# Performance work log

Measured on AMD Instinct MI355X. Metric: run time of the kernel, lower is better.

## Reference

```python
import jax, jax.numpy as jnp
import numpy as np

# static config (matches init_kwargs)
H = 64; W = 64; WS = 8; SHIFT = 4; HEADS = 16; DIM = 512; TED = 512; B = 16
NW = (H // WS) * (W // WS)          # 64 windows
WS2 = WS * WS                        # 64 tokens per window
N = WS2 + 1                          # +1 time-embedding token appended per window
HIDDEN = int(DIM * 4.0)


def _rel_pos_index():
    # standard Swin relative-position index over the WS*WS window tokens
    coords = np.stack(np.meshgrid(np.arange(WS), np.arange(WS), indexing='ij'))  # (2, WS, WS)
    cf = coords.reshape(2, -1)
    rel = (cf[:, :, None] - cf[:, None, :]).transpose(1, 2, 0)  # (WS2, WS2, 2)
    rel[..., 0] += WS - 1
    rel[..., 1] += WS - 1
    rel[..., 0] *= 2 * WS - 1
    return rel.sum(-1)  # (WS2, WS2) int


def _attn_mask():
    # shifted-window attention mask, exactly as built in __init__
    img_mask = np.zeros((H, W), dtype=np.float32)
    slices = (slice(0, -WS), slice(-WS, -SHIFT), slice(-SHIFT, None))
    cnt = 0
    for hs in slices:
        for ws_ in slices:
            img_mask[hs, ws_] = cnt
            cnt += 1
    mw = img_mask.reshape(H // WS, WS, W // WS, WS).transpose(0, 2, 1, 3).reshape(-1, WS2)  # (NW, WS2)
    diff = mw[:, None, :] - mw[:, :, None]
    return np.where(diff != 0, -100.0, 0.0).astype(np.float32)  # (NW, WS2, WS2)


def _ln(x, g, b):
    m = x.mean(-1, keepdims=True)
    v = ((x - m) ** 2).mean(-1, keepdims=True)
    return (x - m) / jnp.sqrt(v + 1e-5) * g + b


def setup_inputs() -> dict:
    key = jax.random.key(0)
    ks = jax.random.split(key, 10)
    s = 0.02
    return {
        'x': jax.random.normal(ks[0], (B, H * W, DIM), dtype=jnp.float32),
        'emb': jax.random.normal(ks[1], (B, TED), dtype=jnp.float32),
        'gamma1': jnp.ones((DIM,), jnp.float32),
        'beta1': jnp.zeros((DIM,), jnp.float32),
        'W_emb': jax.random.normal(ks[2], (TED, DIM), jnp.float32) * s,
        'b_emb': jnp.zeros((DIM,), jnp.float32),
        'W_qkv': jax.random.normal(ks[3], (DIM, 3 * DIM), jnp.float32) * s,
        'b_qkv': jnp.zeros((3 * DIM,), jnp.float32),
        'rel_bias_table': jax.random.normal(ks[4], ((2 * WS - 1) ** 2, HEADS), jnp.float32) * s,
        'W_proj': jax.random.normal(ks[5], (DIM, DIM), jnp.float32) * s,
        'b_proj': jnp.zeros((DIM,), jnp.float32),
        'gamma2': jnp.ones((DIM,), jnp.float32),
        'beta2': jnp.zeros((DIM,), jnp.float32),
        'W1': jax.random.normal(ks[6], (DIM, HIDDEN), jnp.float32) * s,
        'b1': jnp.zeros((HIDDEN,), jnp.float32),
        'W2': jax.random.normal(ks[7], (HIDDEN, DIM), jnp.float32) * s,
        'b2': jnp.zeros((DIM,), jnp.float32),
    }


def reference(x, emb, gamma1, beta1, W_emb, b_emb, W_qkv, b_qkv, rel_bias_table,
              W_proj, b_proj, gamma2, beta2, W1, b1, W2, b2):
    Bb, L, C = x.shape
    hd = C // HEADS
    shortcut = x
    # norm1 -> spatial -> cyclic shift
    xn = _ln(x, gamma1, beta1).reshape(Bb, H, W, C)
    xs = jnp.roll(xn, (-SHIFT, -SHIFT), axis=(1, 2))
    # window partition: (B, NW, WS2, C)
    xw = xs.reshape(Bb, H // WS, WS, W // WS, WS, C).transpose(0, 1, 3, 2, 4, 5)
    xw = xw.reshape(Bb, NW, WS2, C)
    # append time-embedding token to each window
    t = jax.nn.silu(emb) @ W_emb + b_emb                       # (B, C)
    t = jnp.broadcast_to(t[:, None, None, :], (Bb, NW, 1, C))
    xw = jnp.concatenate([xw, t], axis=2).reshape(Bb * NW, N, C)
    # windowed multi-head attention
    qkv = (xw @ W_qkv + b_qkv).reshape(Bb * NW, N, 3, HEADS, hd).transpose(2, 0, 3, 1, 4)
    q, k, v = qkv[0] * (hd ** -0.5), qkv[1], qkv[2]            # (B*NW, HEADS, N, hd)
    attn = jnp.einsum('bhnd,bhmd->bhnm', q, k)
    bias = rel_bias_table[_rel_pos_index().reshape(-1)].reshape(WS2, WS2, HEADS).transpose(2, 0, 1)
    bias = jnp.pad(bias, ((0, 0), (0, 1), (0, 1)))             # zero bias for time token
    attn = attn + bias[None]
    mask = jnp.pad(jnp.asarray(_attn_mask()), ((0, 0), (0, 1), (0, 1)))  # (NW, N, N)
    attn = attn.reshape(Bb, NW, HEADS, N, N) + mask[None, :, None]
    attn = jax.nn.softmax(attn.reshape(Bb * NW, HEADS, N, N), axis=-1)
    out = jnp.einsum('bhnm,bhmd->bnhd', attn, v).reshape(Bb * NW, N, C)
    out = (out @ W_proj + b_proj)[:, :WS2]                     # drop time token
    # window reverse + reverse shift
    out = out.reshape(Bb, H // WS, W // WS, WS, WS, C).transpose(0, 1, 3, 2, 4, 5).reshape(Bb, H, W, C)
    out = jnp.roll(out, (SHIFT, SHIFT), axis=(1, 2)).reshape(Bb, L, C)
    x1 = shortcut + out
    # norm2 + MLP (exact GELU, as torch nn.GELU default)
    hmid = jax.nn.gelu(_ln(x1, gamma2, beta2) @ W1 + b1, approximate=False)
    return x1 + hmid @ W2 + b2
```

## Files before the change

kernel.cpp:

```cpp
#include <hip/hip_runtime.h>
#include <hip/hip_bf16.h>

typedef __hip_bfloat16 bf16;
typedef short short4_t __attribute__((ext_vector_type(4)));
typedef short short8 __attribute__((ext_vector_type(8)));
typedef float f32x4 __attribute__((ext_vector_type(4)));

#define DIMC 512
#define HEADS_ 16
#define NTOK 65
#define NWIN 64
#define NB 16
#define HID 2048
#define TOTROWS 66560
#define IMGROWS 65536
#define ATT_CHUNK_WB 128
#define ATT_CHUNK_ROWS (ATT_CHUNK_WB * NTOK)


__device__ __forceinline__ float b2f(short s) {
  unsigned int u = ((unsigned int)(unsigned short)s) << 16;
  float f; __builtin_memcpy(&f, &u, 4); return f;
}
__device__ __forceinline__ short f2s(float f) {
  bf16 b = __float2bfloat16(f);
  short s; __builtin_memcpy(&s, &b, 2); return s;
}

__device__ __forceinline__ void async_lds16(const bf16* g, bf16* l) {
  __builtin_amdgcn_global_load_lds(
      (const __attribute__((address_space(1))) unsigned int*)g,
      (__attribute__((address_space(3))) unsigned int*)l,
      16, 0, 0);
}

__device__ __forceinline__ void wave_stats512(const float* v, float& m, float& rstd)
{
  float s = 0.0f, ss = 0.0f;
  #pragma unroll
  for (int e = 0; e < 8; ++e) { s += v[e]; ss += v[e] * v[e]; }
  #pragma unroll
  for (int o = 1; o < 64; o <<= 1) { s += __shfl_xor(s, o); ss += __shfl_xor(ss, o); }
  m = s * (1.0f / 512.0f);
  rstd = rsqrtf(ss * (1.0f / 512.0f) - m * m + 1e-5f);
}

__device__ __forceinline__ float gelu_t(float v) {
  float v2 = v * v;
  float a  = fmaf(0.044715f, v2, 1.0f);
  float e  = __builtin_exp2f(-2.3022042f * (v * a));
  return v * __builtin_amdgcn_rcpf(1.0f + e);
}


__global__ __launch_bounds__(256) void time_emb_kernel(
    const float* __restrict__ emb, const float* __restrict__ W_emb,
    const float* __restrict__ b_emb, float* __restrict__ t)
{
  int b = blockIdx.x;
  int c = blockIdx.y * 256 + threadIdx.x;
  __shared__ float se[512];
  for (int k = threadIdx.x; k < 512; k += 256) {
    float e = emb[b * 512 + k];
    se[k] = e / (1.0f + expf(-e));
  }
  __syncthreads();
  float acc = b_emb[c];
  for (int k = 0; k < 512; ++k) acc += se[k] * W_emb[k * 512 + c];
  t[b * 512 + c] = acc;
}

__global__ void transpose_cast_kernel(const float* __restrict__ W, bf16* __restrict__ Wt,
                                      int Kd, int Nd)
{
  __shared__ float tile[32][33];
  int n0 = blockIdx.x * 32, k0 = blockIdx.y * 32;
  for (int r = threadIdx.y; r < 32; r += 8)
    tile[r][threadIdx.x] = W[(long)(k0 + r) * Nd + n0 + threadIdx.x];
  __syncthreads();
  for (int r = threadIdx.y; r < 32; r += 8)
    Wt[(long)(n0 + r) * Kd + k0 + threadIdx.x] = __float2bfloat16(tile[threadIdx.x][r]);
}

__global__ __launch_bounds__(256) void bias_mask_kernel(
    const float* __restrict__ btab, float* __restrict__ tbl)
{
  int h = blockIdx.x, wt = blockIdx.y;
  for (int idx = threadIdx.x; idx < 6400; idx += 256) {
    int i = idx / 80, t = idx % 80;
    float v;
    if (t >= 65) v = -1e30f;
    else if (i >= 64 || t == 64) v = 0.0f;
    else {
      int rel = (((i >> 3) - (t >> 3) + 7) * 15) + ((i & 7) - (t & 7) + 7);
      v = btab[rel * HEADS_ + h];
      int rci = (wt & 2) ? (((i >> 3) < 4) ? 1 : 2) : 0;
      int cci = (wt & 1) ? (((i & 7) < 4) ? 1 : 2) : 0;
      int rct = (wt & 2) ? (((t >> 3) < 4) ? 1 : 2) : 0;
      int cct = (wt & 1) ? (((t & 7) < 4) ? 1 : 2) : 0;
      if (rci * 3 + cci != rct * 3 + cct) v -= 100.0f;
    }
    tbl[(h * 4 + wt) * 6400 + idx] = v;
  }
}

__global__ __launch_bounds__(256) void ln1_window_kernel(
    const float* __restrict__ x, const float* __restrict__ gamma,
    const float* __restrict__ beta, const float* __restrict__ t,
    bf16* __restrict__ xw)
{
  long r = (long)blockIdx.x * 4 + (threadIdx.x >> 6);
  int lane = threadIdx.x & 63;
  int wb = (int)(r / NTOK), i = (int)(r % NTOK);
  int b = wb >> 6, w = wb & 63;
  bf16* out = xw + r * 512 + lane * 8;
  if (i == 64) {
    const float* tr = t + b * 512 + lane * 8;
    short8 o;
    #pragma unroll
    for (int e = 0; e < 8; ++e) o[e] = f2s(tr[e]);
    *(short8*)out = o;
    return;
  }
  int wh = w >> 3, ww = w & 7, ih = i >> 3, iw = i & 7;
  int hsrc = ((wh * 8 + ih) + 4) & 63;
  int wsrc = ((ww * 8 + iw) + 4) & 63;
  const float* xr = x + ((long)b * 4096 + hsrc * 64 + wsrc) * 512 + lane * 8;
  float v[8];
  *(f32x4*)&v[0] = *(const f32x4*)xr;
  *(f32x4*)&v[4] = *(const f32x4*)(xr + 4);
  float m, rstd;
  wave_stats512(v, m, rstd);
  const float* g = gamma + lane * 8;
  const float* bt = beta + lane * 8;
  short8 o;
  #pragma unroll
  for (int e = 0; e < 8; ++e) o[e] = f2s((v[e] - m) * rstd * g[e] + bt[e]);
  *(short8*)out = o;
}

__global__ __launch_bounds__(256) void ln2_kernel(
    const bf16* __restrict__ x1, const float* __restrict__ gamma,
    const float* __restrict__ beta, bf16* __restrict__ out)
{
  long r = (long)blockIdx.x * 4 + (threadIdx.x >> 6);
  int lane = threadIdx.x & 63;
  short8 xv = *(const short8*)(x1 + r * 512 + lane * 8);
  float v[8];
  #pragma unroll
  for (int e = 0; e < 8; ++e) v[e] = b2f(xv[e]);
  float m, rstd;
  wave_stats512(v, m, rstd);
  const float* g = gamma + lane * 8;
  const float* bt = beta + lane * 8;
  short8 o;
  #pragma unroll
  for (int e = 0; e < 8; ++e) o[e] = f2s((v[e] - m) * rstd * g[e] + bt[e]);
  *(short8*)(out + r * 512 + lane * 8) = o;
}

template<int EPI, int K>
__global__ __launch_bounds__(256, 3) void gemmk_kernel(
    const bf16* __restrict__ A, const bf16* __restrict__ Bt,
    const float* __restrict__ bias, int N, int nx,
    bf16* __restrict__ outB, float* __restrict__ outF,
    const float* __restrict__ xinF, const bf16* __restrict__ xinB, int rowOffset)
{
  constexpr int NKT = K / 32;
  static_assert((NKT - 1) % 3 == 0, "triplet peel needs NKT = 3m+1");
  __shared__ bf16 ldsbuf[6 * 128 * 32];
  bf16* const lAp = ldsbuf;
  bf16* const lBp = ldsbuf + 3 * 4096;
  const int tid = threadIdx.x;
  const int lane = tid & 63, wv = tid >> 6;
  const int wm = wv >> 1, wn = wv & 1;
  const int fr = lane & 15, fg = lane >> 4;

  const int nwg = gridDim.x, bid = blockIdx.x;
  const int q8 = nwg >> 3, rr8 = nwg & 7;
  const int xcd = bid & 7, idx = bid >> 3;
  const int sid = (xcd < rr8 ? xcd * (q8 + 1) : rr8 * (q8 + 1) + (xcd - rr8) * q8) + idx;
  const long row0 = (long)(sid / nx) * 128;
  const long col0 = (long)(sid % nx) * 128;

  const int rl = lane >> 2, sp = lane & 3;
  const int s = sp ^ ((rl >> 1) & 3);
  const bf16* ga0 = A  + (row0 + wv * 32 + rl) * (long)K + s * 8;
  const bf16* ga1 = ga0 + 16 * (long)K;
  const bf16* gb0 = Bt + (col0 + wv * 32 + rl) * (long)K + s * 8;
  const bf16* gb1 = gb0 + 16 * (long)K;

  f32x4 acc[4][4] = {};
  const int swr = (fg ^ ((fr >> 1) & 3)) << 4;

  auto stage = [&](int buf, int t) {
    const long o = (long)t * 32;
    async_lds16(ga0 + o, &lAp[buf * 4096 + (wv * 32) * 32]);
    async_lds16(ga1 + o, &lAp[buf * 4096 + (wv * 32 + 16) * 32]);
    async_lds16(gb0 + o, &lBp[buf * 4096 + (wv * 32) * 32]);
    async_lds16(gb1 + o, &lBp[buf * 4096 + (wv * 32 + 16) * 32]);
  };

  stage(0, 0);
  stage(1, 1);

#define GBODY(BUF)                                                              \
  do {                                                                          \
    if (t + 1 < NKT) asm volatile("s_waitcnt vmcnt(4)" ::: "memory");           \
    else             asm volatile("s_waitcnt vmcnt(0)" ::: "memory");           \
    __builtin_amdgcn_s_barrier();                                               \
    short8 bfv[4], af[4];                                                       \
    _Pragma("unroll")                                                           \
    for (int ni = 0; ni < 4; ++ni)                                              \
      bfv[ni] = *(const short8*)((const char*)&lBp[(BUF) * 4096] +              \
                                 (wn * 64 + ni * 16 + fr) * 64 + swr);          \
    _Pragma("unroll")                                                           \
    for (int mi = 0; mi < 4; ++mi)                                              \
      af[mi] = *(const short8*)((const char*)&lAp[(BUF) * 4096] +               \
                                (wm * 64 + mi * 16 + fr) * 64 + swr);           \
    if (t + 2 < NKT) stage(((BUF) + 2) % 3, t + 2);                             \
    __builtin_amdgcn_s_setprio(1);                                              \
    _Pragma("unroll")                                                           \
    for (int mi = 0; mi < 4; ++mi)                                              \
      _Pragma("unroll")                                                         \
      for (int ni = 0; ni < 4; ++ni)                                            \
        acc[mi][ni] = __builtin_amdgcn_mfma_f32_16x16x32_bf16(                  \
            af[mi], bfv[ni], acc[mi][ni], 0, 0, 0);                             \
    __builtin_amdgcn_s_setprio(0);                                              \
    ++t;                                                                        \
  } while (0)

  int t = 0;
  GBODY(0);
  for (int g = 0; g < (NKT - 1) / 3; ++g) {
    GBODY(1);
    GBODY(2);
    GBODY(0);
  }
#undef GBODY

  if (EPI == 2 || EPI == 3) {
    __syncthreads();
    float* ep = (float*)ldsbuf;
    const int l31 = lane & 31, lr2 = lane >> 5;
    const f32x4 b4 = *(const f32x4*)&bias[col0 + l31 * 4];
    #pragma unroll
    for (int h = 0; h < 2; ++h) {
      if (wm == h) {
        #pragma unroll
        for (int mi = 0; mi < 4; ++mi)
          #pragma unroll
          for (int ni = 0; ni < 4; ++ni)
            #pragma unroll
            for (int j = 0; j < 4; ++j)
              ep[(mi * 16 + fg * 4 + j) * 132 + wn * 64 + ni * 16 + fr] = acc[mi][ni][j];
      }
      __syncthreads();
      #pragma unroll
      for (int it = 0; it < 8; ++it) {
        int lrow = it * 8 + wv * 2 + lr2;
        long rr = row0 + h * 64 + lrow;
        f32x4 v = *(const f32x4*)&ep[lrow * 132 + l31 * 4];
        v += b4;
        if (EPI == 2) {
          int grow = rowOffset + (int)rr;
          int ii = grow % NTOK;
          if (ii != 64) {
            int wb = grow / NTOK;
            int b = wb >> 6, w = wb & 63;
            int wh = w >> 3, ww = w & 7, ih = ii >> 3, iw = ii & 7;
            int hh   = ((wh * 8 + ih) + 4) & 63;
            int wcol = ((ww * 8 + iw) + 4) & 63;
            long o = ((long)b * 4096 + hh * 64 + wcol) * 512 + col0 + l31 * 4;
            f32x4 xi = *(const f32x4*)&xinF[o];
            f32x4 x1 = xi + v;
            short4_t s4;
            #pragma unroll
            for (int e = 0; e < 4; ++e) s4[e] = f2s(x1[e]);
            *(short4_t*)&outB[o] = s4;
          }
        } else {
          long o = rr * N + col0 + l31 * 4;
          short4_t xv = *(const short4_t*)&xinB[o];
          f32x4 xf;
          #pragma unroll
          for (int e = 0; e < 4; ++e) xf[e] = b2f(xv[e]);
          *(f32x4*)&outF[o] = xf + v;
        }
      }
      __syncthreads();
    }
    return;
  }

  float bs[4];
  #pragma unroll
  for (int ni = 0; ni < 4; ++ni) bs[ni] = bias[col0 + wn * 64 + ni * 16 + fr];
  #pragma unroll
  for (int mi = 0; mi < 4; ++mi) {
    #pragma unroll
    for (int j = 0; j < 4; ++j) {
      long rr = row0 + wm * 64 + mi * 16 + fg * 4 + j;
      #pragma unroll
      for (int ni = 0; ni < 4; ++ni) {
        long cc = col0 + wn * 64 + ni * 16 + fr;
        float v = acc[mi][ni][j] + bs[ni];
        if (EPI == 0) {
          outB[rr * N + cc] = __float2bfloat16(v);
        } else {
          outB[rr * N + cc] = __float2bfloat16(gelu_t(v));
        }
      }
    }
  }
}

__global__ __launch_bounds__(64, 2) void attn_mfma_kernel(
    const bf16* __restrict__ qkv, bf16* __restrict__ attnO,
    const float* __restrict__ tbl, int wb0)
{
  __shared__ bf16 P[80 * 104];
  const int lwb = blockIdx.x, h = blockIdx.y;
  const int lane = threadIdx.x;
  const int fr = lane & 15, g = lane >> 4;
  const float scale = 0.17677669529663687f;
  const bf16* base = qkv + (long)lwb * 65 * 1536 + h * 32 + g * 8;

  for (int idx = lane; idx < 240; idx += 64) {
    int i = idx / 3, sl = idx % 3;
    *(short8*)&P[i * 104 + 80 + sl * 8] = (short8){0, 0, 0, 0, 0, 0, 0, 0};
  }

  short8 bq[5];
  #pragma unroll
  for (int tn = 0; tn < 5; ++tn) {
    int qr = tn * 16 + fr; qr = qr > 64 ? 64 : qr;
    bq[tn] = *(const short8*)(base + (long)qr * 1536);
  }

  f32x4 acc[5][5];
  #pragma unroll
  for (int tm = 0; tm < 5; ++tm) {
    int kr = tm * 16 + fr; kr = kr > 64 ? 64 : kr;
    short8 ak = *(const short8*)(base + 512 + (long)kr * 1536);
    #pragma unroll
    for (int tn = 0; tn < 5; ++tn)
      acc[tm][tn] = __builtin_amdgcn_mfma_f32_16x16x32_bf16(
          ak, bq[tn], (f32x4){0.0f, 0.0f, 0.0f, 0.0f}, 0, 0, 0);
  }

  const int w = (wb0 + lwb) & 63;
  const int wt = (((w >> 3) == 7) ? 2 : 0) + (((w & 7) == 7) ? 1 : 0);
  const float* tp = tbl + (h * 4 + wt) * 6400;
  #pragma unroll
  for (int tn = 0; tn < 5; ++tn) {
    const int i = tn * 16 + fr;
    const float* ti = tp + i * 80 + g * 4;
    float m = -3.0e38f;
    #pragma unroll
    for (int tm = 0; tm < 5; ++tm) {
      f32x4 bv = *(const f32x4*)(ti + tm * 16);
      #pragma unroll
      for (int r = 0; r < 4; ++r) {
        float sv = fmaf(acc[tm][tn][r], scale, bv[r]);
        acc[tm][tn][r] = sv;
        m = fmaxf(m, sv);
      }
    }
    m = fmaxf(m, __shfl_xor(m, 16));
    m = fmaxf(m, __shfl_xor(m, 32));
    float l = 0.0f;
    #pragma unroll
    for (int tm = 0; tm < 5; ++tm)
      #pragma unroll
      for (int r = 0; r < 4; ++r) {
        float e = __expf(acc[tm][tn][r] - m);
        acc[tm][tn][r] = e;
        l += e;
      }
    l += __shfl_xor(l, 16);
    l += __shfl_xor(l, 32);
    float inv = 1.0f / l;
    #pragma unroll
    for (int tm = 0; tm < 5; ++tm) {
      short4_t pk;
      #pragma unroll
      for (int r = 0; r < 4; ++r) pk[r] = f2s(acc[tm][tn][r] * inv);
      *(short4_t*)&P[i * 104 + tm * 16 + g * 4] = pk;
    }
  }

  const bf16* vbase = qkv + (long)lwb * 65 * 1536 + 1024 + h * 32;
  f32x4 oacc[2][5] = {};
  #pragma unroll
  for (int kt = 0; kt < 3; ++kt) {
    short8 bp[5];
    #pragma unroll
    for (int tn = 0; tn < 5; ++tn)
      bp[tn] = *(const short8*)&P[(tn * 16 + fr) * 104 + kt * 32 + g * 8];
    #pragma unroll
    for (int ma = 0; ma < 2; ++ma) {
      short8 av;
      #pragma unroll
      for (int e = 0; e < 8; ++e) {
        int vr = kt * 32 + g * 8 + e; vr = vr > 64 ? 64 : vr;
        av[e] = *(const short*)(vbase + (long)vr * 1536 + ma * 16 + fr);
      }
      #pragma unroll
      for (int tn = 0; tn < 5; ++tn)
        oacc[ma][tn] = __builtin_amdgcn_mfma_f32_16x16x32_bf16(
            av, bp[tn], oacc[ma][tn], 0, 0, 0);
    }
  }

  #pragma unroll
  for (int tn = 0; tn < 5; ++tn) {
    int i = tn * 16 + fr;
    if (i < 65) {
      bf16* op = attnO + (long)(lwb * 65 + i) * 512 + h * 32 + g * 4;
      #pragma unroll
      for (int ma = 0; ma < 2; ++ma) {
        short4_t o4;
        #pragma unroll
        for (int r = 0; r < 4; ++r) o4[r] = f2s(oacc[ma][tn][r]);
        *(short4_t*)(op + ma * 16) = o4;
      }
    }
  }
}


extern "C" void kernel_launch(void* const* d_in, const int* in_sizes, int n_in,
                              void* d_out, int out_size, void* d_ws, size_t ws_size,
                              hipStream_t stream)
{
  const float* x      = (const float*)d_in[0];
  const float* emb    = (const float*)d_in[1];
  const float* gamma1 = (const float*)d_in[2];
  const float* beta1  = (const float*)d_in[3];
  const float* W_emb  = (const float*)d_in[4];
  const float* b_emb  = (const float*)d_in[5];
  const float* W_qkv  = (const float*)d_in[6];
  const float* b_qkv  = (const float*)d_in[7];
  const float* btab   = (const float*)d_in[8];
  const float* W_proj = (const float*)d_in[9];
  const float* b_proj = (const float*)d_in[10];
  const float* gamma2 = (const float*)d_in[11];
  const float* beta2  = (const float*)d_in[12];
  const float* W1     = (const float*)d_in[13];
  const float* b1     = (const float*)d_in[14];
  const float* W2     = (const float*)d_in[15];
  const float* b2     = (const float*)d_in[16];
  float* out = (float*)d_out;
  (void)n_in; (void)in_sizes; (void)out_size;

  char* ws = (char*)d_ws;
  size_t off = 0;
  auto alloc = [&](size_t bytes) -> char* {
    char* p = ws + off;
    off += (bytes + 255) & ~(size_t)255;
    return p;
  };
  bf16* wt_qkv  = (bf16*)alloc((size_t)1536 * 512 * 2);
  bf16* wt_proj = (bf16*)alloc((size_t)512 * 512 * 2);
  bf16* wt1     = (bf16*)alloc((size_t)2048 * 512 * 2);
  bf16* wt2     = (bf16*)alloc((size_t)512 * 2048 * 2);
  float* tvec   = (float*)alloc((size_t)16 * 512 * 4);
  float* tbl    = (float*)alloc((size_t)16 * 4 * 6400 * 4);

  const size_t sz_xw    = (size_t)TOTROWS * 512 * 2;
  const size_t sz_qkv   = (size_t)TOTROWS * 1536 * 2;
  const size_t sz_attnO = (size_t)TOTROWS * 512 * 2;
  const bool big = ws_size >= off + sz_xw + sz_qkv + sz_attnO + (4u << 20);

  transpose_cast_kernel<<<dim3(1536 / 32, 512 / 32), dim3(32, 8), 0, stream>>>(W_qkv, wt_qkv, 512, 1536);
  transpose_cast_kernel<<<dim3(512 / 32, 512 / 32),  dim3(32, 8), 0, stream>>>(W_proj, wt_proj, 512, 512);
  transpose_cast_kernel<<<dim3(2048 / 32, 512 / 32), dim3(32, 8), 0, stream>>>(W1, wt1, 512, 2048);
  transpose_cast_kernel<<<dim3(512 / 32, 2048 / 32), dim3(32, 8), 0, stream>>>(W2, wt2, 2048, 512);
  time_emb_kernel<<<dim3(16, 2), 256, 0, stream>>>(emb, W_emb, b_emb, tvec);
  bias_mask_kernel<<<dim3(16, 4), 256, 0, stream>>>(btab, tbl);

  if (big) {
    char* regionA = alloc(sz_xw);
    char* regionQ = alloc(sz_qkv);
    bf16* attnO   = (bf16*)alloc(sz_attnO);
    bf16* xw   = (bf16*)regionA;
    bf16* x1b  = (bf16*)regionA;
    bf16* qkv  = (bf16*)regionQ;
    bf16* h_c  = (bf16*)regionQ;
    bf16* ln2b = (bf16*)(regionQ + (size_t)32768 * 2048 * 2);

    ln1_window_kernel<<<TOTROWS / 4, 256, 0, stream>>>(x, gamma1, beta1, tvec, xw);
    gemmk_kernel<0, 512><<<12 * 520, 256, 0, stream>>>(
        xw, wt_qkv, b_qkv, 1536, 12, qkv, nullptr, nullptr, nullptr, 0);
    attn_mfma_kernel<<<dim3(NB * NWIN, HEADS_), 64, 0, stream>>>(qkv, attnO, tbl, 0);
    gemmk_kernel<2, 512><<<4 * 520, 256, 0, stream>>>(
        attnO, wt_proj, b_proj, 512, 4, x1b, nullptr, x, nullptr, 0);
    ln2_kernel<<<IMGROWS / 4, 256, 0, stream>>>(x1b, gamma2, beta2, ln2b);
    for (int mc = 0; mc < 2; ++mc) {
      long r0 = (long)mc * 32768;
      gemmk_kernel<1, 512><<<16 * 256, 256, 0, stream>>>(
          ln2b + r0 * 512, wt1, b1, 2048, 16, h_c, nullptr, nullptr, nullptr, 0);
      gemmk_kernel<3, 2048><<<4 * 256, 256, 0, stream>>>(
          h_c, wt2, b2, 512, 4, nullptr, out + r0 * 512, nullptr, x1b + r0 * 512, 0);
    }
  } else {
    char* regionA = alloc(sz_xw);
    bf16* xw   = (bf16*)regionA;
    bf16* x1b  = (bf16*)regionA;
    bf16* qkv_c = (bf16*)alloc((size_t)ATT_CHUNK_ROWS * 1536 * 2);
    char* regionB = alloc(sz_attnO);
    bf16* attnO = (bf16*)regionB;
    bf16* ln2b  = (bf16*)regionB;
    bf16* h_c   = (bf16*)alloc((size_t)16384 * 2048 * 2);

    ln1_window_kernel<<<TOTROWS / 4, 256, 0, stream>>>(x, gamma1, beta1, tvec, xw);
    for (int ac = 0; ac < 8; ++ac) {
      long r0 = (long)ac * ATT_CHUNK_ROWS;
      gemmk_kernel<0, 512><<<12 * 65, 256, 0, stream>>>(
          xw + r0 * 512, wt_qkv, b_qkv, 1536, 12, qkv_c, nullptr, nullptr, nullptr, 0);
      attn_mfma_kernel<<<dim3(ATT_CHUNK_WB, HEADS_), 64, 0, stream>>>(
          qkv_c, attnO + r0 * 512, tbl, ac * ATT_CHUNK_WB);
    }
    gemmk_kernel<2, 512><<<4 * 520, 256, 0, stream>>>(
        attnO, wt_proj, b_proj, 512, 4, x1b, nullptr, x, nullptr, 0);
    ln2_kernel<<<IMGROWS / 4, 256, 0, stream>>>(x1b, gamma2, beta2, ln2b);
    for (int mc = 0; mc < 4; ++mc) {
      long r0 = (long)mc * 16384;
      gemmk_kernel<1, 512><<<16 * 128, 256, 0, stream>>>(
          ln2b + r0 * 512, wt1, b1, 2048, 16, h_c, nullptr, nullptr, nullptr, 0);
      gemmk_kernel<3, 2048><<<4 * 128, 256, 0, stream>>>(
          h_c, wt2, b2, 512, 4, nullptr, out + r0 * 512, nullptr, x1b + r0 * 512, 0);
    }
  }
}
```

Measured before the change: 822.2 us.

## Stage EPI0/1 outputs through LDS for vectorized stores; bf16 shortcut copy

The GEMM epilogue for the QKV and MLP1 outputs now adds bias and GELU in registers, stages the tile through LDS, and writes 16-byte bf16 vectors instead of scattered 2-byte stores. The LN1 kernel also writes a bf16 copy of x into the output buffer, and the projection epilogue reads that as the residual instead of fp32 x, halving the residual read. The bf16 residual adds rounding error to x1, and reusing the output buffer as scratch is safe only because MLP2 overwrites it afterwards. The extra LN1 write adds traffic.

```diff
diff --git a/kernel.cpp b/kernel.cpp
--- a/kernel.cpp
+++ b/kernel.cpp
@@ -107,7 +107,7 @@
 __global__ __launch_bounds__(256) void ln1_window_kernel(
     const float* __restrict__ x, const float* __restrict__ gamma,
     const float* __restrict__ beta, const float* __restrict__ t,
-    bf16* __restrict__ xw)
+    bf16* __restrict__ xw, bf16* __restrict__ xb)
 {
   long r = (long)blockIdx.x * 4 + (threadIdx.x >> 6);
   int lane = threadIdx.x & 63;
@@ -125,10 +125,15 @@
   int wh = w >> 3, ww = w & 7, ih = i >> 3, iw = i & 7;
   int hsrc = ((wh * 8 + ih) + 4) & 63;
   int wsrc = ((ww * 8 + iw) + 4) & 63;
-  const float* xr = x + ((long)b * 4096 + hsrc * 64 + wsrc) * 512 + lane * 8;
+  long src = (long)b * 4096 + hsrc * 64 + wsrc;
+  const float* xr = x + src * 512 + lane * 8;
   float v[8];
   *(f32x4*)&v[0] = *(const f32x4*)xr;
   *(f32x4*)&v[4] = *(const f32x4*)(xr + 4);
+  short8 xo;
+  #pragma unroll
+  for (int e = 0; e < 8; ++e) xo[e] = f2s(v[e]);
+  *(short8*)(xb + src * 512 + lane * 8) = xo;
   float m, rstd;
   wave_stats512(v, m, rstd);
   const float* g = gamma + lane * 8;
@@ -164,7 +169,7 @@
     const bf16* __restrict__ A, const bf16* __restrict__ Bt,
     const float* __restrict__ bias, int N, int nx,
     bf16* __restrict__ outB, float* __restrict__ outF,
-    const float* __restrict__ xinF, const bf16* __restrict__ xinB, int rowOffset)
+    const bf16* __restrict__ xinB, int rowOffset)
 {
   constexpr int NKT = K / 32;
   static_assert((NKT - 1) % 3 == 0, "triplet peel needs NKT = 3m+1");
@@ -239,29 +244,45 @@
   }
 #undef GBODY
 
-  if (EPI == 2 || EPI == 3) {
+  __syncthreads();
+  float* ep = (float*)ldsbuf;
+  float bs[4];
+  #pragma unroll
+  for (int ni = 0; ni < 4; ++ni) bs[ni] = bias[col0 + wn * 64 + ni * 16 + fr];
+  const int l31 = lane & 31, lr2 = lane >> 5;
+  const int c16 = tid & 15, r16 = tid >> 4;
+  #pragma unroll
+  for (int h = 0; h < 2; ++h) {
+    if (wm == h) {
+      #pragma unroll
+      for (int mi = 0; mi < 4; ++mi)
+        #pragma unroll
+        for (int ni = 0; ni < 4; ++ni)
+          #pragma unroll
+          for (int j = 0; j < 4; ++j) {
+            float v = acc[mi][ni][j] + bs[ni];
+            if (EPI == 1) v = gelu_t(v);
+            ep[(mi * 16 + fg * 4 + j) * 132 + wn * 64 + ni * 16 + fr] = v;
+          }
+    }
     __syncthreads();
-    float* ep = (float*)ldsbuf;
-    const int l31 = lane & 31, lr2 = lane >> 5;
-    const f32x4 b4 = *(const f32x4*)&bias[col0 + l31 * 4];
-    #pragma unroll
-    for (int h = 0; h < 2; ++h) {
-      if (wm == h) {
+    if (EPI == 0 || EPI == 1) {
+      #pragma unroll
+      for (int it = 0; it < 4; ++it) {
+        int lrow = it * 16 + r16;
+        f32x4 a = *(const f32x4*)&ep[lrow * 132 + c16 * 8];
+        f32x4 bq = *(const f32x4*)&ep[lrow * 132 + c16 * 8 + 4];
+        short8 o8;
         #pragma unroll
-        for (int mi = 0; mi < 4; ++mi)
-          #pragma unroll
-          for (int ni = 0; ni < 4; ++ni)
-            #pragma unroll
-            for (int j = 0; j < 4; ++j)
-              ep[(mi * 16 + fg * 4 + j) * 132 + wn * 64 + ni * 16 + fr] = acc[mi][ni][j];
+        for (int e = 0; e < 4; ++e) { o8[e] = f2s(a[e]); o8[4 + e] = f2s(bq[e]); }
+        *(short8*)&outB[(row0 + h * 64 + lrow) * N + col0 + c16 * 8] = o8;
       }
-      __syncthreads();
+    } else {
       #pragma unroll
       for (int it = 0; it < 8; ++it) {
         int lrow = it * 8 + wv * 2 + lr2;
         long rr = row0 + h * 64 + lrow;
         f32x4 v = *(const f32x4*)&ep[lrow * 132 + l31 * 4];
-        v += b4;
         if (EPI == 2) {
           int grow = rowOffset + (int)rr;
           int ii = grow % NTOK;
@@ -272,11 +293,10 @@
             int hh   = ((wh * 8 + ih) + 4) & 63;
             int wcol = ((ww * 8 + iw) + 4) & 63;
             long o = ((long)b * 4096 + hh * 64 + wcol) * 512 + col0 + l31 * 4;
-            f32x4 xi = *(const f32x4*)&xinF[o];
-            f32x4 x1 = xi + v;
+            short4_t xv = *(const short4_t*)&xinB[o];
             short4_t s4;
             #pragma unroll
-            for (int e = 0; e < 4; ++e) s4[e] = f2s(x1[e]);
+            for (int e = 0; e < 4; ++e) s4[e] = f2s(b2f(xv[e]) + v[e]);
             *(short4_t*)&outB[o] = s4;
           }
         } else {
@@ -288,30 +308,8 @@
           *(f32x4*)&outF[o] = xf + v;
         }
       }
-      __syncthreads();
-    }
-    return;
-  }
-
-  float bs[4];
-  #pragma unroll
-  for (int ni = 0; ni < 4; ++ni) bs[ni] = bias[col0 + wn * 64 + ni * 16 + fr];
-  #pragma unroll
-  for (int mi = 0; mi < 4; ++mi) {
-    #pragma unroll
-    for (int j = 0; j < 4; ++j) {
-      long rr = row0 + wm * 64 + mi * 16 + fg * 4 + j;
-      #pragma unroll
-      for (int ni = 0; ni < 4; ++ni) {
-        long cc = col0 + wn * 64 + ni * 16 + fr;
-        float v = acc[mi][ni][j] + bs[ni];
-        if (EPI == 0) {
-          outB[rr * N + cc] = __float2bfloat16(v);
-        } else {
-          outB[rr * N + cc] = __float2bfloat16(gelu_t(v));
-        }
-      }
-    }
+    }
+    __syncthreads();
   }
 }
 
@@ -454,6 +452,8 @@
   float* out = (float*)d_out;
   (void)n_in; (void)in_sizes; (void)out_size;
 
+  bf16* xb = (bf16*)out;
+
   char* ws = (char*)d_ws;
   size_t off = 0;
   auto alloc = [&](size_t bytes) -> char* {
@@ -490,19 +490,19 @@
     bf16* h_c  = (bf16*)regionQ;
     bf16* ln2b = (bf16*)(regionQ + (size_t)32768 * 2048 * 2);
 
-    ln1_window_kernel<<<TOTROWS / 4, 256, 0, stream>>>(x, gamma1, beta1, tvec, xw);
+    ln1_window_kernel<<<TOTROWS / 4, 256, 0, stream>>>(x, gamma1, beta1, tvec, xw, xb);
     gemmk_kernel<0, 512><<<12 * 520, 256, 0, stream>>>(
-        xw, wt_qkv, b_qkv, 1536, 12, qkv, nullptr, nullptr, nullptr, 0);
+        xw, wt_qkv, b_qkv, 1536, 12, qkv, nullptr, nullptr, 0);
     attn_mfma_kernel<<<dim3(NB * NWIN, HEADS_), 64, 0, stream>>>(qkv, attnO, tbl, 0);
     gemmk_kernel<2, 512><<<4 * 520, 256, 0, stream>>>(
-        attnO, wt_proj, b_proj, 512, 4, x1b, nullptr, x, nullptr, 0);
+        attnO, wt_proj, b_proj, 512, 4, x1b, nullptr, xb, 0);
     ln2_kernel<<<IMGROWS / 4, 256, 0, stream>>>(x1b, gamma2, beta2, ln2b);
     for (int mc = 0; mc < 2; ++mc) {
       long r0 = (long)mc * 32768;
       gemmk_kernel<1, 512><<<16 * 256, 256, 0, stream>>>(
-          ln2b + r0 * 512, wt1, b1, 2048, 16, h_c, nullptr, nullptr, nullptr, 0);
+          ln2b + r0 * 512, wt1, b1, 2048, 16, h_c, nullptr, nullptr, 0);
       gemmk_kernel<3, 2048><<<4 * 256, 256, 0, stream>>>(
-          h_c, wt2, b2, 512, 4, nullptr, out + r0 * 512, nullptr, x1b + r0 * 512, 0);
+          h_c, wt2, b2, 512, 4, nullptr, out + r0 * 512, x1b + r0 * 512, 0);
     }
   } else {
     char* regionA = alloc(sz_xw);
@@ -514,23 +514,23 @@
     bf16* ln2b  = (bf16*)regionB;
     bf16* h_c   = (bf16*)alloc((size_t)16384 * 2048 * 2);
 
-    ln1_window_kernel<<<TOTROWS / 4, 256, 0, stream>>>(x, gamma1, beta1, tvec, xw);
+    ln1_window_kernel<<<TOTROWS / 4, 256, 0, stream>>>(x, gamma1, beta1, tvec, xw, xb);
     for (int ac = 0; ac < 8; ++ac) {
       long r0 = (long)ac * ATT_CHUNK_ROWS;
       gemmk_kernel<0, 512><<<12 * 65, 256, 0, stream>>>(
-          xw + r0 * 512, wt_qkv, b_qkv, 1536, 12, qkv_c, nullptr, nullptr, nullptr, 0);
+          xw + r0 * 512, wt_qkv, b_qkv, 1536, 12, qkv_c, nullptr, nullptr, 0);
       attn_mfma_kernel<<<dim3(ATT_CHUNK_WB, HEADS_), 64, 0, stream>>>(
           qkv_c, attnO + r0 * 512, tbl, ac * ATT_CHUNK_WB);
     }
     gemmk_kernel<2, 512><<<4 * 520, 256, 0, stream>>>(
-        attnO, wt_proj, b_proj, 512, 4, x1b, nullptr, x, nullptr, 0);
+        attnO, wt_proj, b_proj, 512, 4, x1b, nullptr, xb, 0);
     ln2_kernel<<<IMGROWS / 4, 256, 0, stream>>>(x1b, gamma2, beta2, ln2b);
     for (int mc = 0; mc < 4; ++mc) {
       long r0 = (long)mc * 16384;
       gemmk_kernel<1, 512><<<16 * 128, 256, 0, stream>>>(
-          ln2b + r0 * 512, wt1, b1, 2048, 16, h_c, nullptr, nullptr, nullptr, 0);
+          ln2b + r0 * 512, wt1, b1, 2048, 16, h_c, nullptr, nullptr, 0);
       gemmk_kernel<3, 2048><<<4 * 128, 256, 0, stream>>>(
-          h_c, wt2, b2, 512, 4, nullptr, out + r0 * 512, nullptr, x1b + r0 * 512, 0);
-    }
-  }
-}
+          h_c, wt2, b2, 512, 4, nullptr, out + r0 * 512, x1b + r0 * 512, 0);
+    }
+  }
+}
```

Result: slower. 849.1 us (+3.3%).

## Add 256x256-tile 8-wave GEMM with ping-pong LDS pipeline for all big-path GEMMs

Applied to the files above, without the earlier changes.

Introduces a new GEMM kernel using 512-thread workgroups computing 256x256 output tiles, with 64-wide K steps, double-buffered LDS split into half-tiles, XOR-swizzled LDS layout, and staggered async loads between MFMA phases using s_setprio. It also remaps block IDs across the 8 XCDs so neighbouring tiles share an XCD. All four GEMMs on the big path switch to it, with grids resized. Larger tiles raise arithmetic intensity and cut global traffic, but at one workgroup per CU, which lowers occupancy and makes tail effects coarser.

```diff
diff --git a/kernel.cpp b/kernel.cpp
--- a/kernel.cpp
+++ b/kernel.cpp
@@ -157,6 +157,206 @@
   #pragma unroll
   for (int e = 0; e < 8; ++e) o[e] = f2s((v[e] - m) * rstd * g[e] + bt[e]);
   *(short8*)(out + r * 512 + lane * 8) = o;
+}
+
+template<int EPI, int K>
+__global__ __launch_bounds__(512, 1) void gemm8p_kernel(
+    const bf16* __restrict__ A, const bf16* __restrict__ Bt,
+    const float* __restrict__ bias, int N, int nx,
+    bf16* __restrict__ outB, float* __restrict__ outF,
+    const float* __restrict__ xinF, const bf16* __restrict__ xinB, int rowOffset)
+{
+  constexpr int NKT = K / 64;
+  __shared__ bf16 lds[8][128 * 64];
+  const int tid = threadIdx.x;
+  const int lane = tid & 63, wv = tid >> 6;
+  const int wm = wv >> 2, wn = wv & 3;
+  const int fr = lane & 15, fg = lane >> 4;
+
+  const int nwg = gridDim.x, bid = blockIdx.x;
+  const int q8 = nwg >> 3, rr8 = nwg & 7;
+  const int xcd = bid & 7, idx = bid >> 3;
+  const int sid = (xcd < rr8 ? xcd * (q8 + 1) : rr8 * (q8 + 1) + (xcd - rr8) * q8) + idx;
+  const long row0 = (long)(sid / nx) * 256;
+  const long col0 = (long)(sid % nx) * 256;
+
+  const int rl = lane >> 3, sl = lane & 7;
+  const int sls = sl ^ rl;
+
+  auto stageH = [&](int buf, int mat, int h, int kt) {
+    const bf16* base = mat ? Bt : A;
+    const long rb = (mat ? col0 : row0) + h * 128 + wv * 8 + rl;
+    const bf16* src = base + rb * (long)K + kt + sls * 8;
+    bf16* dst = &lds[buf * 4 + mat * 2 + h][(wv * 8) * 64];
+    async_lds16(src, dst);
+    async_lds16(src + 64 * (long)K, dst + 64 * 64);
+  };
+  auto fragA = [&](int buf, int h, int mi, int ks) -> short8 {
+    int r = wm * 64 + mi * 16 + fr;
+    return *(const short8*)((const char*)&lds[buf * 4 + h][0] + r * 128 + (((ks * 4 + fg) ^ (r & 7)) << 4));
+  };
+  auto fragB = [&](int buf, int h, int ni, int ks) -> short8 {
+    int r = wn * 32 + ni * 16 + fr;
+    return *(const short8*)((const char*)&lds[buf * 4 + 2 + h][0] + r * 128 + (((ks * 4 + fg) ^ (r & 7)) << 4));
+  };
+
+  f32x4 acc[8][4] = {};
+  short8 af[4][2], bv[2][2];
+
+  stageH(0, 0, 0, 0); stageH(0, 1, 0, 0); stageH(0, 1, 1, 0); stageH(0, 0, 1, 0);
+
+  for (int t = 0; t < NKT; ++t) {
+    const int buf = t & 1, nb = buf ^ 1;
+    const bool st = (t + 1 < NKT);
+    const int kt2 = (t + 1) << 6;
+
+    asm volatile("s_waitcnt vmcnt(4)" ::: "memory");
+    __builtin_amdgcn_s_barrier();
+    #pragma unroll
+    for (int mi = 0; mi < 4; ++mi) { af[mi][0] = fragA(buf, 0, mi, 0); af[mi][1] = fragA(buf, 0, mi, 1); }
+    #pragma unroll
+    for (int ni = 0; ni < 2; ++ni) { bv[ni][0] = fragB(buf, 0, ni, 0); bv[ni][1] = fragB(buf, 0, ni, 1); }
+    if (st) stageH(nb, 0, 0, kt2);
+    __builtin_amdgcn_s_setprio(1);
+    #pragma unroll
+    for (int mi = 0; mi < 4; ++mi)
+      #pragma unroll
+      for (int ni = 0; ni < 2; ++ni)
+        #pragma unroll
+        for (int ks = 0; ks < 2; ++ks)
+          acc[mi][ni] = __builtin_amdgcn_mfma_f32_16x16x32_bf16(af[mi][ks], bv[ni][ks], acc[mi][ni], 0, 0, 0);
+    __builtin_amdgcn_s_setprio(0);
+
+    if (st) asm volatile("s_waitcnt vmcnt(4)" ::: "memory");
+    else    asm volatile("s_waitcnt vmcnt(2)" ::: "memory");
+    __builtin_amdgcn_s_barrier();
+    #pragma unroll
+    for (int ni = 0; ni < 2; ++ni) { bv[ni][0] = fragB(buf, 1, ni, 0); bv[ni][1] = fragB(buf, 1, ni, 1); }
+    if (st) stageH(nb, 1, 0, kt2);
+    __builtin_amdgcn_s_setprio(1);
+    #pragma unroll
+    for (int mi = 0; mi < 4; ++mi)
+      #pragma unroll
+      for (int ni = 0; ni < 2; ++ni)
+        #pragma unroll
+        for (int ks = 0; ks < 2; ++ks)
+          acc[mi][2 + ni] = __builtin_amdgcn_mfma_f32_16x16x32_bf16(af[mi][ks], bv[ni][ks], acc[mi][2 + ni], 0, 0, 0);
+    __builtin_amdgcn_s_setprio(0);
+
+    if (st) asm volatile("s_waitcnt vmcnt(4)" ::: "memory");
+    else    asm volatile("s_waitcnt vmcnt(0)" ::: "memory");
+    __builtin_amdgcn_s_barrier();
+    #pragma unroll
+    for (int mi = 0; mi < 4; ++mi) { af[mi][0] = fragA(buf, 1, mi, 0); af[mi][1] = fragA(buf, 1, mi, 1); }
+    #pragma unroll
+    for (int ni = 0; ni < 2; ++ni) { bv[ni][0] = fragB(buf, 0, ni, 0); bv[ni][1] = fragB(buf, 0, ni, 1); }
+    if (st) stageH(nb, 1, 1, kt2);
+    __builtin_amdgcn_s_setprio(1);
+    #pragma unroll
+    for (int mi = 0; mi < 4; ++mi)
+      #pragma unroll
+      for (int ni = 0; ni < 2; ++ni)
+        #pragma unroll
+        for (int ks = 0; ks < 2; ++ks)
+          acc[4 + mi][ni] = __builtin_amdgcn_mfma_f32_16x16x32_bf16(af[mi][ks], bv[ni][ks], acc[4 + mi][ni], 0, 0, 0);
+    __builtin_amdgcn_s_setprio(0);
+
+    __builtin_amdgcn_s_barrier();
+    #pragma unroll
+    for (int ni = 0; ni < 2; ++ni) { bv[ni][0] = fragB(buf, 1, ni, 0); bv[ni][1] = fragB(buf, 1, ni, 1); }
+    if (st) stageH(nb, 0, 1, kt2);
+    __builtin_amdgcn_s_setprio(1);
+    #pragma unroll
+    for (int mi = 0; mi < 4; ++mi)
+      #pragma unroll
+      for (int ni = 0; ni < 2; ++ni)
+        #pragma unroll
+        for (int ks = 0; ks < 2; ++ks)
+          acc[4 + mi][2 + ni] = __builtin_amdgcn_mfma_f32_16x16x32_bf16(af[mi][ks], bv[ni][ks], acc[4 + mi][2 + ni], 0, 0, 0);
+    __builtin_amdgcn_s_setprio(0);
+  }
+
+  if (EPI == 0 || EPI == 1) {
+    float bs[2][2];
+    #pragma unroll
+    for (int nh = 0; nh < 2; ++nh)
+      #pragma unroll
+      for (int ni = 0; ni < 2; ++ni)
+        bs[nh][ni] = bias[col0 + nh * 128 + wn * 32 + ni * 16 + fr];
+    #pragma unroll
+    for (int h = 0; h < 2; ++h)
+      #pragma unroll
+      for (int mi = 0; mi < 4; ++mi)
+        #pragma unroll
+        for (int j = 0; j < 4; ++j) {
+          long rr = row0 + h * 128 + wm * 64 + mi * 16 + fg * 4 + j;
+          #pragma unroll
+          for (int nh = 0; nh < 2; ++nh)
+            #pragma unroll
+            for (int ni = 0; ni < 2; ++ni) {
+              long cc = col0 + nh * 128 + wn * 32 + ni * 16 + fr;
+              float v = acc[h * 4 + mi][nh * 2 + ni][j] + bs[nh][ni];
+              if (EPI == 1) v = gelu_t(v);
+              outB[rr * N + cc] = __float2bfloat16(v);
+            }
+        }
+    return;
+  }
+
+  __syncthreads();
+  float* ep = (float*)&lds[0][0];
+  const int c64 = tid & 63, r8 = tid >> 6;
+  const f32x4 b4 = *(const f32x4*)&bias[col0 + c64 * 4];
+  #pragma unroll
+  for (int g = 0; g < 4; ++g) {
+    int h = g >> 1, wmg = g & 1;
+    if (wm == wmg) {
+      #pragma unroll
+      for (int mi = 0; mi < 4; ++mi)
+        #pragma unroll
+        for (int nh = 0; nh < 2; ++nh)
+          #pragma unroll
+          for (int ni = 0; ni < 2; ++ni)
+            #pragma unroll
+            for (int j = 0; j < 4; ++j)
+              ep[(mi * 16 + fg * 4 + j) * 260 + nh * 128 + wn * 32 + ni * 16 + fr] =
+                  acc[h * 4 + mi][nh * 2 + ni][j];
+    }
+    __syncthreads();
+    #pragma unroll
+    for (int it = 0; it < 8; ++it) {
+      int lrow = it * 8 + r8;
+      long rr = row0 + h * 128 + wmg * 64 + lrow;
+      f32x4 v = *(const f32x4*)&ep[lrow * 260 + c64 * 4];
+      v += b4;
+      if (EPI == 2) {
+        int grow = rowOffset + (int)rr;
+        int ii = grow % NTOK;
+        if (ii != 64) {
+          int wb = grow / NTOK;
+          int b = wb >> 6, w = wb & 63;
+          int wh = w >> 3, ww = w & 7, ih = ii >> 3, iw = ii & 7;
+          int hh   = ((wh * 8 + ih) + 4) & 63;
+          int wcol = ((ww * 8 + iw) + 4) & 63;
+          long o = ((long)b * 4096 + hh * 64 + wcol) * 512 + col0 + c64 * 4;
+          f32x4 xi = *(const f32x4*)&xinF[o];
+          f32x4 x1 = xi + v;
+          short4_t s4;
+          #pragma unroll
+          for (int e = 0; e < 4; ++e) s4[e] = f2s(x1[e]);
+          *(short4_t*)&outB[o] = s4;
+        }
+      } else {
+        long o = rr * N + col0 + c64 * 4;
+        short4_t xv = *(const short4_t*)&xinB[o];
+        f32x4 xf;
+        #pragma unroll
+        for (int e = 0; e < 4; ++e) xf[e] = b2f(xv[e]);
+        *(f32x4*)&outF[o] = xf + v;
+      }
+    }
+    __syncthreads();
+  }
 }
 
 template<int EPI, int K>
@@ -359,10 +559,10 @@
     float m = -3.0e38f;
     #pragma unroll
     for (int tm = 0; tm < 5; ++tm) {
-      f32x4 bv = *(const f32x4*)(ti + tm * 16);
+      f32x4 bvv = *(const f32x4*)(ti + tm * 16);
       #pragma unroll
       for (int r = 0; r < 4; ++r) {
-        float sv = fmaf(acc[tm][tn][r], scale, bv[r]);
+        float sv = fmaf(acc[tm][tn][r], scale, bvv[r]);
         acc[tm][tn][r] = sv;
         m = fmaxf(m, sv);
       }
@@ -491,18 +691,18 @@
     bf16* ln2b = (bf16*)(regionQ + (size_t)32768 * 2048 * 2);
 
     ln1_window_kernel<<<TOTROWS / 4, 256, 0, stream>>>(x, gamma1, beta1, tvec, xw);
-    gemmk_kernel<0, 512><<<12 * 520, 256, 0, stream>>>(
-        xw, wt_qkv, b_qkv, 1536, 12, qkv, nullptr, nullptr, nullptr, 0);
+    gemm8p_kernel<0, 512><<<6 * 260, 512, 0, stream>>>(
+        xw, wt_qkv, b_qkv, 1536, 6, qkv, nullptr, nullptr, nullptr, 0);
     attn_mfma_kernel<<<dim3(NB * NWIN, HEADS_), 64, 0, stream>>>(qkv, attnO, tbl, 0);
-    gemmk_kernel<2, 512><<<4 * 520, 256, 0, stream>>>(
-        attnO, wt_proj, b_proj, 512, 4, x1b, nullptr, x, nullptr, 0);
+    gemm8p_kernel<2, 512><<<2 * 260, 512, 0, stream>>>(
+        attnO, wt_proj, b_proj, 512, 2, x1b, nullptr, x, nullptr, 0);
     ln2_kernel<<<IMGROWS / 4, 256, 0, stream>>>(x1b, gamma2, beta2, ln2b);
     for (int mc = 0; mc < 2; ++mc) {
       long r0 = (long)mc * 32768;
-      gemmk_kernel<1, 512><<<16 * 256, 256, 0, stream>>>(
-          ln2b + r0 * 512, wt1, b1, 2048, 16, h_c, nullptr, nullptr, nullptr, 0);
-      gemmk_kernel<3, 2048><<<4 * 256, 256, 0, stream>>>(
-          h_c, wt2, b2, 512, 4, nullptr, out + r0 * 512, nullptr, x1b + r0 * 512, 0);
+      gemm8p_kernel<1, 512><<<8 * 128, 512, 0, stream>>>(
+          ln2b + r0 * 512, wt1, b1, 2048, 8, h_c, nullptr, nullptr, nullptr, 0);
+      gemm8p_kernel<3, 2048><<<2 * 128, 512, 0, stream>>>(
+          h_c, wt2, b2, 512, 2, nullptr, out + r0 * 512, nullptr, x1b + r0 * 512, 0);
     }
   } else {
     char* regionA = alloc(sz_xw);
```

Result: faster. 782.0 us (-4.9%).
